# Kernel tuning notes

Hardware: AMD Instinct MI355X
Metric: run time of the kernel (lower is better)

The kernel has to match this reference:

```python
import jax, jax.numpy as jnp
import numpy as np

NEG_SLOPE = 0.2


def gat_layer(x, src, dst, W, att_src, att_dst, bias, n_nodes):
    # PyG GATConv (heads=1): h = x @ W; per-edge logit = LeakyReLU(a_src.h[src] + a_dst.h[dst]);
    # softmax over edges grouped by destination node; out[d] = sum alpha * h[src] + bias.
    h = x @ W                                  # [N, F]
    a_s = h @ att_src                          # [N]
    a_d = h @ att_dst                          # [N]
    e = a_s[src] + a_d[dst]                    # [E]
    e = jnp.where(e > 0, e, NEG_SLOPE * e)     # leaky_relu
    m = jax.ops.segment_max(e, dst, num_segments=n_nodes)   # [N]
    w = jnp.exp(e - m[dst])                    # [E]
    z = jax.ops.segment_sum(w, dst, num_segments=n_nodes)   # [N]
    alpha = w / z[dst]                         # [E] (self-loops guarantee z>0)
    out = jax.ops.segment_sum(alpha[:, None] * h[src], dst, num_segments=n_nodes)
    return out + bias


def setup_inputs() -> dict:
    key = jax.random.key(0)
    ks = jax.random.split(key, 10)
    N, E, C_IN, H1, H2 = 100000, 3200000, 128, 50, 40
    x = jax.random.normal(ks[0], (N, C_IN), dtype=jnp.float32)
    edge_index = jax.random.randint(ks[1], (2, E), 0, N, dtype=jnp.int64)
    g1 = 1.0 / np.sqrt(C_IN)
    g2 = 1.0 / np.sqrt(H1)
    return {
        "x": x,
        "edge_index": edge_index,
        "W1": jax.random.normal(ks[2], (C_IN, H1), dtype=jnp.float32) * g1,
        "att_src1": jax.random.normal(ks[3], (H1,), dtype=jnp.float32) * g2,
        "att_dst1": jax.random.normal(ks[4], (H1,), dtype=jnp.float32) * g2,
        "bias1": jnp.zeros((H1,), dtype=jnp.float32),
        "W2": jax.random.normal(ks[5], (H1, H2), dtype=jnp.float32) * g2,
        "att_src2": jax.random.normal(ks[6], (H2,), dtype=jnp.float32) / np.sqrt(H2),
        "att_dst2": jax.random.normal(ks[7], (H2,), dtype=jnp.float32) / np.sqrt(H2),
        "bias2": jnp.zeros((H2,), dtype=jnp.float32),
    }


def reference(x, edge_index, W1, att_src1, att_dst1, bias1, W2, att_src2, att_dst2, bias2):
    n_nodes = x.shape[0]
    # PyG GATConv default add_self_loops=True: append (i, i) for every node.
    loop = jnp.arange(n_nodes, dtype=edge_index.dtype)
    src = jnp.concatenate([edge_index[0], loop])
    dst = jnp.concatenate([edge_index[1], loop])
    h = jax.nn.relu(gat_layer(x, src, dst, W1, att_src1, att_dst1, bias1, n_nodes))
    h = jax.nn.relu(gat_layer(h, src, dst, W2, att_src2, att_dst2, bias2, n_nodes))
    return h, edge_index
```

## Files before the change

kernel.cpp:

```cpp
#include <hip/hip_runtime.h>
#include <hip/hip_bf16.h>
#include <math.h>

#define NEG_SLOPE 0.2f
#define RBITS 8
#define RNODES 256
#define CHUNK 8192
#define CAP   9216
#define HS    32


__device__ __forceinline__ float waveReduceSum(float v) {
    #pragma unroll
    for (int off = 32; off > 0; off >>= 1) v += __shfl_xor(v, off);
    return v;
}

__device__ __forceinline__ unsigned pack_bf16(float a, float b) {
    __hip_bfloat162 p(__float2bfloat16(a), __float2bfloat16(b));
    return *reinterpret_cast<unsigned*>(&p);
}
__device__ __forceinline__ float bf16lo_f(unsigned u) { return __uint_as_float(u << 16); }
__device__ __forceinline__ float bf16hi_f(unsigned u) { return __uint_as_float(u & 0xFFFF0000u); }


__global__ void prep(const float* __restrict__ W1, float* __restrict__ WT1,
                     const float* __restrict__ W2, float* __restrict__ WT2,
                     int* __restrict__ bcursor,
                     int K1, int F1, int KP1, int FP1,
                     int K2, int F2, int KP2, int FP2, int NB) {
    int i = blockIdx.x * blockDim.x + threadIdx.x;
    int z1 = FP1 * KP1, z2 = FP2 * KP2;
    if (i < z1) {
        int f = i / KP1, k = i - f * KP1;
        WT1[i] = (f < F1 && k < K1) ? W1[k * F1 + f] : 0.f;
    } else if (i < z1 + z2) {
        int j = i - z1;
        int f = j / KP2, k = j - f * KP2;
        WT2[j] = (f < F2 && k < K2) ? W2[k * F2 + f] : 0.f;
    } else if (i < z1 + z2 + NB) {
        bcursor[i - z1 - z2] = 0;
    }
}


__global__ __launch_bounds__(512) void binning(
        const int* __restrict__ src, const int* __restrict__ dst,
        int* __restrict__ bcursor, int* __restrict__ binned,
        long E, int N, long TOT) {
    __shared__ int hist[512];
    __shared__ int base[512];
    int t = threadIdx.x;
    hist[t] = 0;
    __syncthreads();
    long c0 = blockIdx.x * (long)CHUNK;
    long c1 = c0 + CHUNK; if (c1 > TOT) c1 = TOT;
    for (long i = c0 + t; i < c1; i += 512) {
        int d = (i < E) ? dst[i] : (int)(i - E);
        atomicAdd(&hist[d >> RBITS], 1);
    }
    __syncthreads();
    {
        int c = hist[t];
        base[t] = c ? atomicAdd(&bcursor[t], c) : 0;
        hist[t] = 0;
    }
    __syncthreads();
    for (long i = c0 + t; i < c1; i += 512) {
        int s, d;
        if (i < E) { s = src[i]; d = dst[i]; } else { s = d = (int)(i - E); }
        int b = d >> RBITS;
        int p = base[b] + atomicAdd(&hist[b], 1);
        if (p >= CAP) p = CAP - 1;
        binned[(long)b * CAP + p] = ((d & (RNODES - 1)) << 17) | s;
    }
}

__global__ __launch_bounds__(512) void bucket_scan(
        const int* __restrict__ bcursor, int* __restrict__ bstarts,
        int* __restrict__ starts, int NB, int N, int TOT) {
    __shared__ int s[512];
    int t = threadIdx.x;
    int v = (t < NB) ? bcursor[t] : 0;
    s[t] = v;
    __syncthreads();
    for (int off = 1; off < 512; off <<= 1) {
        int u = (t >= off) ? s[t - off] : 0;
        __syncthreads();
        s[t] += u;
        __syncthreads();
    }
    int excl = s[t] - v;
    if (t < NB) bstarts[t] = excl;
    if (t == 0) { bstarts[NB] = TOT; starts[N] = TOT; }
}

__global__ __launch_bounds__(512) void bucket_csr(
        const int* __restrict__ binned, const int* __restrict__ bstarts,
        int* __restrict__ starts, int* __restrict__ csr_src, int N) {
    __shared__ int cnt[RNODES];
    __shared__ int scn[RNODES];
    int b = blockIdx.x, t = threadIdx.x;
    int node0 = b << RBITS;
    int R = N - node0; if (R > RNODES) R = RNODES;
    int e0 = bstarts[b];
    int ecnt = bstarts[b + 1] - e0;
    const int* bin = binned + (long)b * CAP;
    if (t < RNODES) cnt[t] = 0;
    __syncthreads();
    for (int i = t; i < ecnt; i += 512)
        atomicAdd(&cnt[bin[i] >> 17], 1);
    __syncthreads();
    int v = (t < RNODES) ? cnt[t] : 0;
    if (t < RNODES) scn[t] = v;
    __syncthreads();
    for (int off = 1; off < RNODES; off <<= 1) {
        int u = (t >= off && t < RNODES) ? scn[t - off] : 0;
        __syncthreads();
        if (t < RNODES) scn[t] += u;
        __syncthreads();
    }
    if (t < RNODES) {
        int excl = scn[t] - v;
        if (t < R) starts[node0 + t] = e0 + excl;
        cnt[t] = excl;
    }
    __syncthreads();
    for (int i = t; i < ecnt; i += 512) {
        int packed = bin[i];
        int ld = packed >> 17;
        int p = atomicAdd(&cnt[ld], 1);
        csr_src[e0 + p] = packed & 0x1FFFF;
    }
}

template <int K, int KP, int F, int FPH>
__global__ __launch_bounds__(512) void gemm_tile(
        const float* __restrict__ x, const float* __restrict__ WT,
        const float* __restrict__ att_s, const float* __restrict__ att_d,
        unsigned* __restrict__ hb, float* __restrict__ as_, float* __restrict__ ad_,
        int N) {
    __shared__ float xT[KP * 65];
    __shared__ float asl[64], adl[64];
    int t = threadIdx.x;
    int lane = t & 63;
    int w = t >> 6;
    long n0 = (long)blockIdx.x * 64;
    int n = (int)n0 + lane;

    if (t < 64) { asl[t] = 0.f; adl[t] = 0.f; }
    for (int idx = t; idx < KP * 64; idx += 512) {
        int nn = idx / KP, k = idx - nn * KP;
        float v = 0.f;
        if (k < K && n0 + nn < N) v = x[(n0 + nn) * (long)K + k];
        xT[k * 65 + nn] = v;
    }
    __syncthreads();

    int f0 = __builtin_amdgcn_readfirstlane(w * 8);
    float acc[8] = {0.f, 0.f, 0.f, 0.f, 0.f, 0.f, 0.f, 0.f};
    if (f0 < F) {
        const float* wbase = WT + (long)f0 * KP;
        for (int k0 = 0; k0 < KP; k0 += 4) {
            float x0 = xT[(k0 + 0) * 65 + lane];
            float x1 = xT[(k0 + 1) * 65 + lane];
            float x2 = xT[(k0 + 2) * 65 + lane];
            float x3 = xT[(k0 + 3) * 65 + lane];
            #pragma unroll
            for (int j = 0; j < 8; ++j) {
                const float* wr = wbase + j * KP + k0;
                float a = acc[j];
                a = fmaf(wr[0], x0, a);
                a = fmaf(wr[1], x1, a);
                a = fmaf(wr[2], x2, a);
                a = fmaf(wr[3], x3, a);
                acc[j] = a;
            }
        }
        float ps = 0.f, pd = 0.f;
        #pragma unroll
        for (int j = 0; j < 8; ++j) {
            float sa = (f0 + j < F) ? att_s[f0 + j] : 0.f;
            float da = (f0 + j < F) ? att_d[f0 + j] : 0.f;
            ps = fmaf(acc[j], sa, ps);
            pd = fmaf(acc[j], da, pd);
        }
        atomicAdd(&asl[lane], ps);
        atomicAdd(&adl[lane], pd);
    }
    __syncthreads();

    if (f0 < F && n < N) {
        int f0h = f0 >> 1;
        #pragma unroll
        for (int q = 0; q < 4; ++q) {
            int fp = f0h + q;
            if (fp < FPH) hb[(long)n * HS + fp] = pack_bf16(acc[2 * q], acc[2 * q + 1]);
        }
    }
    if (w == 0 && n < N) { as_[n] = asl[lane]; ad_[n] = adl[lane]; }
}

template <int F>
__global__ __launch_bounds__(256) void gat_gather(
                           const int* __restrict__ csr_src, const int* __restrict__ starts,
                           const float* __restrict__ as_, const float* __restrict__ ad_,
                           const unsigned* __restrict__ hb, const float* __restrict__ bias,
                           float* __restrict__ out, int N) {
    constexpr int NU4 = (F + 7) / 8;
    int lane = threadIdx.x & 63;
    int g  = lane >> 3;
    int fl = lane & 7;
    bool actf = (fl < NU4);
    long wave = (blockIdx.x * (long)blockDim.x + threadIdx.x) >> 6;
    if (wave >= N) return;
    int d = (int)wave;
    int s0 = starts[d], s1 = starts[d + 1];
    float add = ad_[d];
    const unsigned* hbase = hb + 4 * fl;

    float lsum = 0.f;
    float a0 = 0.f, a1 = 0.f, a2 = 0.f, a3 = 0.f;
    float a4 = 0.f, a5 = 0.f, a6 = 0.f, a7 = 0.f;

    for (int base = s0; base < s1; base += 64) {
        int k = base + lane;
        int s = (k < s1) ? csr_src[k] : 0;
        unsigned soff = (unsigned)s << 5;
        float e = as_[s] + add;
        e = e > 0.f ? e : NEG_SLOPE * e;
        float w = (k < s1) ? __expf(e) : 0.f;
        lsum += w;
        int cnt = min(64, s1 - base);
        int nst = (cnt + 7) >> 3;
        int j = 0;
        for (; j + 4 <= nst; j += 4) {
            int i0 = 8 * j + g;
            unsigned so0 = __shfl(soff, i0);
            unsigned so1 = __shfl(soff, i0 + 8);
            unsigned so2 = __shfl(soff, i0 + 16);
            unsigned so3 = __shfl(soff, i0 + 24);
            uint4 h0 = make_uint4(0u,0u,0u,0u), h1 = h0, h2 = h0, h3 = h0;
            if (actf) {
                h0 = *(const uint4*)(hbase + so0);
                h1 = *(const uint4*)(hbase + so1);
                h2 = *(const uint4*)(hbase + so2);
                h3 = *(const uint4*)(hbase + so3);
            }
            float w0 = __shfl(w, i0);
            float w1 = __shfl(w, i0 + 8);
            float w2 = __shfl(w, i0 + 16);
            float w3 = __shfl(w, i0 + 24);
            a0 = fmaf(w0, bf16lo_f(h0.x), a0); a1 = fmaf(w0, bf16hi_f(h0.x), a1);
            a2 = fmaf(w0, bf16lo_f(h0.y), a2); a3 = fmaf(w0, bf16hi_f(h0.y), a3);
            a4 = fmaf(w0, bf16lo_f(h0.z), a4); a5 = fmaf(w0, bf16hi_f(h0.z), a5);
            a6 = fmaf(w0, bf16lo_f(h0.w), a6); a7 = fmaf(w0, bf16hi_f(h0.w), a7);
            a0 = fmaf(w1, bf16lo_f(h1.x), a0); a1 = fmaf(w1, bf16hi_f(h1.x), a1);
            a2 = fmaf(w1, bf16lo_f(h1.y), a2); a3 = fmaf(w1, bf16hi_f(h1.y), a3);
            a4 = fmaf(w1, bf16lo_f(h1.z), a4); a5 = fmaf(w1, bf16hi_f(h1.z), a5);
            a6 = fmaf(w1, bf16lo_f(h1.w), a6); a7 = fmaf(w1, bf16hi_f(h1.w), a7);
            a0 = fmaf(w2, bf16lo_f(h2.x), a0); a1 = fmaf(w2, bf16hi_f(h2.x), a1);
            a2 = fmaf(w2, bf16lo_f(h2.y), a2); a3 = fmaf(w2, bf16hi_f(h2.y), a3);
            a4 = fmaf(w2, bf16lo_f(h2.z), a4); a5 = fmaf(w2, bf16hi_f(h2.z), a5);
            a6 = fmaf(w2, bf16lo_f(h2.w), a6); a7 = fmaf(w2, bf16hi_f(h2.w), a7);
            a0 = fmaf(w3, bf16lo_f(h3.x), a0); a1 = fmaf(w3, bf16hi_f(h3.x), a1);
            a2 = fmaf(w3, bf16lo_f(h3.y), a2); a3 = fmaf(w3, bf16hi_f(h3.y), a3);
            a4 = fmaf(w3, bf16lo_f(h3.z), a4); a5 = fmaf(w3, bf16hi_f(h3.z), a5);
            a6 = fmaf(w3, bf16lo_f(h3.w), a6); a7 = fmaf(w3, bf16hi_f(h3.w), a7);
        }
        for (; j < nst; ++j) {
            int idx = 8 * j + g;
            float wp = __shfl(w, idx);
            unsigned so = __shfl(soff, idx);
            if (actf) {
                uint4 hv = *(const uint4*)(hbase + so);
                a0 = fmaf(wp, bf16lo_f(hv.x), a0); a1 = fmaf(wp, bf16hi_f(hv.x), a1);
                a2 = fmaf(wp, bf16lo_f(hv.y), a2); a3 = fmaf(wp, bf16hi_f(hv.y), a3);
                a4 = fmaf(wp, bf16lo_f(hv.z), a4); a5 = fmaf(wp, bf16hi_f(hv.z), a5);
                a6 = fmaf(wp, bf16lo_f(hv.w), a6); a7 = fmaf(wp, bf16hi_f(hv.w), a7);
            }
        }
    }

    #pragma unroll
    for (int off = 8; off < 64; off <<= 1) {
        a0 += __shfl_xor(a0, off); a1 += __shfl_xor(a1, off);
        a2 += __shfl_xor(a2, off); a3 += __shfl_xor(a3, off);
        a4 += __shfl_xor(a4, off); a5 += __shfl_xor(a5, off);
        a6 += __shfl_xor(a6, off); a7 += __shfl_xor(a7, off);
    }
    float l = waveReduceSum(lsum);

    if (actf) {
        float inv = 1.f / l;
        int fb = 8 * fl;
        float v[8] = {a0, a1, a2, a3, a4, a5, a6, a7};
        float2* orow = (float2*)(out + (long)d * F + fb);
        #pragma unroll
        for (int i = 0; i < 8; i += 2) {
            if (fb + i < F) {
                float u0 = v[i]     * inv + bias[fb + i];
                float u1 = v[i + 1] * inv + bias[fb + i + 1];
                u0 = u0 > 0.f ? u0 : 0.f;
                u1 = u1 > 0.f ? u1 : 0.f;
                orow[i >> 1] = make_float2(u0, u1);
            }
        }
    }
}

__global__ void copy_edges4(const int4* __restrict__ ei, float4* __restrict__ out, long n4) {
    long i = blockIdx.x * (long)blockDim.x + threadIdx.x;
    if (i < n4) {
        int4 v = ei[i];
        out[i] = make_float4((float)v.x, (float)v.y, (float)v.z, (float)v.w);
    }
}
__global__ void copy_edges_tail(const int* __restrict__ ei, float* __restrict__ out,
                                long lo, long n) {
    long i = lo + blockIdx.x * (long)blockDim.x + threadIdx.x;
    if (i < n) out[i] = (float)ei[i];
}


extern "C" void kernel_launch(void* const* d_in, const int* in_sizes, int n_in,
                              void* d_out, int out_size, void* d_ws, size_t ws_size,
                              hipStream_t stream) {
    const float* x         = (const float*)d_in[0];
    const int*   edge_idx  = (const int*)d_in[1];
    const float* W1        = (const float*)d_in[2];
    const float* att_src1  = (const float*)d_in[3];
    const float* att_dst1  = (const float*)d_in[4];
    const float* bias1     = (const float*)d_in[5];
    const float* W2        = (const float*)d_in[6];
    const float* att_src2  = (const float*)d_in[7];
    const float* att_dst2  = (const float*)d_in[8];
    const float* bias2     = (const float*)d_in[9];

    const int  CIN = 128, F1 = 50, F2 = 40;
    const int  KP1 = 128, FP1 = 56;
    const int  KP2 = 52,  FP2 = 40;
    const int  N = in_sizes[0] / CIN;
    const long E = in_sizes[1] / 2;
    const int* src = edge_idx;
    const int* dst = edge_idx + E;
    const long TOT = E + N;
    const int  NB = (N + RNODES - 1) >> RBITS;

    char* wsb = (char*)d_ws;
    size_t regionA = (size_t)NB * CAP * 4;
    if ((size_t)N * HS * 4 > regionA) regionA = (size_t)N * HS * 4;
    int*      binned = (int*)wsb;
    unsigned* hb     = (unsigned*)wsb;
    float*    hout   = (float*)(wsb + regionA);
    float*    as_    = hout + (long)N * F1;
    float*    ad_    = as_ + N;
    int*      starts  = (int*)(ad_ + N);
    int*      csr_src = starts + (N + 1);
    int*      bstarts = csr_src + TOT;
    int*      bcursor = bstarts + (NB + 1);
    float*    WT1     = (float*)(bcursor + NB + 3);
    float*    WT2     = WT1 + FP1 * KP1;

    float* out_h = (float*)d_out;
    float* out_e = out_h + (long)N * F2;

    const int B = 256;
    const int nodeWaveBlocks = (N + 3) / 4;
    const int nTileBlocks = (N + 63) / 64;
    const int nBinBlocks = (int)((TOT + CHUNK - 1) / CHUNK);
    const int prepElems = FP1 * KP1 + FP2 * KP2 + NB;

    prep<<<dim3((prepElems + B - 1) / B), dim3(B), 0, stream>>>(
        W1, WT1, W2, WT2, bcursor, CIN, F1, KP1, FP1, F1, F2, KP2, FP2, NB);
    binning<<<dim3(nBinBlocks), dim3(512), 0, stream>>>(src, dst, bcursor, binned, E, N, TOT);
    bucket_scan<<<dim3(1), dim3(512), 0, stream>>>(bcursor, bstarts, starts, NB, N, (int)TOT);
    bucket_csr<<<dim3(NB), dim3(512), 0, stream>>>(binned, bstarts, starts, csr_src, N);

    gemm_tile<CIN, KP1, F1, FP1 / 2><<<dim3(nTileBlocks), dim3(512), 0, stream>>>(x, WT1, att_src1, att_dst1, hb, as_, ad_, N);
    gat_gather<F1><<<dim3(nodeWaveBlocks), dim3(B), 0, stream>>>(csr_src, starts, as_, ad_, hb, bias1, hout, N);

    gemm_tile<F1, KP2, F2, FP2 / 2><<<dim3(nTileBlocks), dim3(512), 0, stream>>>(hout, WT2, att_src2, att_dst2, hb, as_, ad_, N);
    gat_gather<F2><<<dim3(nodeWaveBlocks), dim3(B), 0, stream>>>(csr_src, starts, as_, ad_, hb, bias2, out_h, N);

    long n_e = 2 * E;
    long n4  = n_e / 4;
    copy_edges4<<<dim3((int)((n4 + B - 1) / B)), dim3(B), 0, stream>>>((const int4*)edge_idx, (float4*)out_e, n4);
    if (n_e - n4 * 4 > 0)
        copy_edges_tail<<<dim3(1), dim3(B), 0, stream>>>(edge_idx, out_e, n4 * 4, n_e);
}
```

Measured before the change: 406.5 us.

## Precompute edge weights in separate pass, shrink layer-2 row stride, fuse edge copy into GEMM

```diff
diff --git a/kernel.cpp b/kernel.cpp
--- a/kernel.cpp
+++ b/kernel.cpp
@@ -7,7 +7,8 @@
 #define RNODES 256
 #define CHUNK 8192
 #define CAP   9216
-#define HS    32
+#define HS1   32
+#define HS2   20
 
 
 __device__ __forceinline__ float waveReduceSum(float v) {
@@ -134,12 +135,31 @@
     }
 }
 
-template <int K, int KP, int F, int FPH>
+__global__ __launch_bounds__(256) void edge_w(
+        const int* __restrict__ csr_src, const int* __restrict__ starts,
+        const float* __restrict__ as_, const float* __restrict__ ad_,
+        float* __restrict__ w_, int N) {
+    long wave = (blockIdx.x * (long)blockDim.x + threadIdx.x) >> 6;
+    int lane = threadIdx.x & 63;
+    if (wave >= N) return;
+    int d = (int)wave;
+    int s0 = starts[d], s1 = starts[d + 1];
+    float add = ad_[d];
+    for (int k = s0 + lane; k < s1; k += 64) {
+        int s = csr_src[k];
+        float e = as_[s] + add;
+        e = e > 0.f ? e : NEG_SLOPE * e;
+        w_[k] = __expf(e);
+    }
+}
+
+template <int K, int KP, int F, int FPH, int HS_, bool DOCOPY>
 __global__ __launch_bounds__(512) void gemm_tile(
         const float* __restrict__ x, const float* __restrict__ WT,
         const float* __restrict__ att_s, const float* __restrict__ att_d,
         unsigned* __restrict__ hb, float* __restrict__ as_, float* __restrict__ ad_,
-        int N) {
+        int N, const int4* __restrict__ ei4, float4* __restrict__ oe4,
+        long q0, long q1) {
     __shared__ float xT[KP * 65];
     __shared__ float asl[64], adl[64];
     int t = threadIdx.x;
@@ -195,16 +215,25 @@
         #pragma unroll
         for (int q = 0; q < 4; ++q) {
             int fp = f0h + q;
-            if (fp < FPH) hb[(long)n * HS + fp] = pack_bf16(acc[2 * q], acc[2 * q + 1]);
+            if (fp < FPH) hb[(long)n * HS_ + fp] = pack_bf16(acc[2 * q], acc[2 * q + 1]);
         }
     }
     if (w == 0 && n < N) { as_[n] = asl[lane]; ad_[n] = adl[lane]; }
-}
-
-template <int F>
+
+    if (DOCOPY) {
+        long gtid = (long)blockIdx.x * blockDim.x + threadIdx.x;
+        long stride = (long)gridDim.x * blockDim.x;
+        for (long i = q0 + gtid; i < q1; i += stride) {
+            int4 v = ei4[i];
+            oe4[i] = make_float4((float)v.x, (float)v.y, (float)v.z, (float)v.w);
+        }
+    }
+}
+
+template <int F, int HS_>
 __global__ __launch_bounds__(256) void gat_gather(
                            const int* __restrict__ csr_src, const int* __restrict__ starts,
-                           const float* __restrict__ as_, const float* __restrict__ ad_,
+                           const float* __restrict__ w_,
                            const unsigned* __restrict__ hb, const float* __restrict__ bias,
                            float* __restrict__ out, int N) {
     constexpr int NU4 = (F + 7) / 8;
@@ -216,7 +245,6 @@
     if (wave >= N) return;
     int d = (int)wave;
     int s0 = starts[d], s1 = starts[d + 1];
-    float add = ad_[d];
     const unsigned* hbase = hb + 4 * fl;
 
     float lsum = 0.f;
@@ -226,10 +254,8 @@
     for (int base = s0; base < s1; base += 64) {
         int k = base + lane;
         int s = (k < s1) ? csr_src[k] : 0;
-        unsigned soff = (unsigned)s << 5;
-        float e = as_[s] + add;
-        e = e > 0.f ? e : NEG_SLOPE * e;
-        float w = (k < s1) ? __expf(e) : 0.f;
+        float w = (k < s1) ? w_[k] : 0.f;
+        unsigned soff = (unsigned)s * HS_;
         lsum += w;
         int cnt = min(64, s1 - base);
         int nst = (cnt + 7) >> 3;
@@ -309,13 +335,6 @@
     }
 }
 
-__global__ void copy_edges4(const int4* __restrict__ ei, float4* __restrict__ out, long n4) {
-    long i = blockIdx.x * (long)blockDim.x + threadIdx.x;
-    if (i < n4) {
-        int4 v = ei[i];
-        out[i] = make_float4((float)v.x, (float)v.y, (float)v.z, (float)v.w);
-    }
-}
 __global__ void copy_edges_tail(const int* __restrict__ ei, float* __restrict__ out,
                                 long lo, long n) {
     long i = lo + blockIdx.x * (long)blockDim.x + threadIdx.x;
@@ -349,7 +368,7 @@
 
     char* wsb = (char*)d_ws;
     size_t regionA = (size_t)NB * CAP * 4;
-    if ((size_t)N * HS * 4 > regionA) regionA = (size_t)N * HS * 4;
+    if ((size_t)N * HS1 * 4 > regionA) regionA = (size_t)N * HS1 * 4;
     int*      binned = (int*)wsb;
     unsigned* hb     = (unsigned*)wsb;
     float*    hout   = (float*)(wsb + regionA);
@@ -357,7 +376,8 @@
     float*    ad_    = as_ + N;
     int*      starts  = (int*)(ad_ + N);
     int*      csr_src = starts + (N + 1);
-    int*      bstarts = csr_src + TOT;
+    float*    w_      = (float*)(csr_src + TOT);
+    int*      bstarts = (int*)(w_ + TOT);
     int*      bcursor = bstarts + (NB + 1);
     float*    WT1     = (float*)(bcursor + NB + 3);
     float*    WT2     = WT1 + FP1 * KP1;
@@ -371,21 +391,28 @@
     const int nBinBlocks = (int)((TOT + CHUNK - 1) / CHUNK);
     const int prepElems = FP1 * KP1 + FP2 * KP2 + NB;
 
+    long n_e  = 2 * E;
+    long n4   = n_e / 4;
+    long qmid = n4 / 2;
+
     prep<<<dim3((prepElems + B - 1) / B), dim3(B), 0, stream>>>(
         W1, WT1, W2, WT2, bcursor, CIN, F1, KP1, FP1, F1, F2, KP2, FP2, NB);
     binning<<<dim3(nBinBlocks), dim3(512), 0, stream>>>(src, dst, bcursor, binned, E, N, TOT);
     bucket_scan<<<dim3(1), dim3(512), 0, stream>>>(bcursor, bstarts, starts, NB, N, (int)TOT);
     bucket_csr<<<dim3(NB), dim3(512), 0, stream>>>(binned, bstarts, starts, csr_src, N);
 
-    gemm_tile<CIN, KP1, F1, FP1 / 2><<<dim3(nTileBlocks), dim3(512), 0, stream>>>(x, WT1, att_src1, att_dst1, hb, as_, ad_, N);
-    gat_gather<F1><<<dim3(nodeWaveBlocks), dim3(B), 0, stream>>>(csr_src, starts, as_, ad_, hb, bias1, hout, N);
-
-    gemm_tile<F1, KP2, F2, FP2 / 2><<<dim3(nTileBlocks), dim3(512), 0, stream>>>(hout, WT2, att_src2, att_dst2, hb, as_, ad_, N);
-    gat_gather<F2><<<dim3(nodeWaveBlocks), dim3(B), 0, stream>>>(csr_src, starts, as_, ad_, hb, bias2, out_h, N);
-
-    long n_e = 2 * E;
-    long n4  = n_e / 4;
-    copy_edges4<<<dim3((int)((n4 + B - 1) / B)), dim3(B), 0, stream>>>((const int4*)edge_idx, (float4*)out_e, n4);
+    gemm_tile<CIN, KP1, F1, FP1 / 2, HS1, true><<<dim3(nTileBlocks), dim3(512), 0, stream>>>(
+        x, WT1, att_src1, att_dst1, hb, as_, ad_, N,
+        (const int4*)edge_idx, (float4*)out_e, 0, qmid);
+    edge_w<<<dim3(nodeWaveBlocks), dim3(B), 0, stream>>>(csr_src, starts, as_, ad_, w_, N);
+    gat_gather<F1, HS1><<<dim3(nodeWaveBlocks), dim3(B), 0, stream>>>(csr_src, starts, w_, hb, bias1, hout, N);
+
+    gemm_tile<F1, KP2, F2, HS2, HS2, true><<<dim3(nTileBlocks), dim3(512), 0, stream>>>(
+        hout, WT2, att_src2, att_dst2, hb, as_, ad_, N,
+        (const int4*)edge_idx, (float4*)out_e, qmid, n4);
+    edge_w<<<dim3(nodeWaveBlocks), dim3(B), 0, stream>>>(csr_src, starts, as_, ad_, w_, N);
+    gat_gather<F2, HS2><<<dim3(nodeWaveBlocks), dim3(B), 0, stream>>>(csr_src, starts, w_, hb, bias2, out_h, N);
+
     if (n_e - n4 * 4 > 0)
         copy_edges_tail<<<dim3(1), dim3(B), 0, stream>>>(edge_idx, out_e, n4 * 4, n_e);
 }
```

Result: slower. 437.1 us (+7.5%).

## Embed source attention score into bf16 feature rows and shrink layer-2 row stride

Applied to the files above, without the earlier changes.

```diff
diff --git a/kernel.cpp b/kernel.cpp
--- a/kernel.cpp
+++ b/kernel.cpp
@@ -7,7 +7,8 @@
 #define RNODES 256
 #define CHUNK 8192
 #define CAP   9216
-#define HS    32
+#define HS1   32
+#define HS2   24
 
 
 __device__ __forceinline__ float waveReduceSum(float v) {
@@ -134,12 +135,13 @@
     }
 }
 
-template <int K, int KP, int F, int FPH>
+template <int K, int KP, int F, int FPH, int HS_>
 __global__ __launch_bounds__(512) void gemm_tile(
         const float* __restrict__ x, const float* __restrict__ WT,
         const float* __restrict__ att_s, const float* __restrict__ att_d,
-        unsigned* __restrict__ hb, float* __restrict__ as_, float* __restrict__ ad_,
+        unsigned* __restrict__ hb, float* __restrict__ ad_,
         int N) {
+    constexpr int ASLOT = 4 * ((F + 7) / 8);
     __shared__ float xT[KP * 65];
     __shared__ float asl[64], adl[64];
     int t = threadIdx.x;
@@ -195,23 +197,28 @@
         #pragma unroll
         for (int q = 0; q < 4; ++q) {
             int fp = f0h + q;
-            if (fp < FPH) hb[(long)n * HS + fp] = pack_bf16(acc[2 * q], acc[2 * q + 1]);
-        }
-    }
-    if (w == 0 && n < N) { as_[n] = asl[lane]; ad_[n] = adl[lane]; }
-}
-
-template <int F>
+            if (fp < FPH) hb[(long)n * HS_ + fp] = pack_bf16(acc[2 * q], acc[2 * q + 1]);
+        }
+    }
+    if (w == 0 && n < N) {
+        hb[(long)n * HS_ + ASLOT] = __float_as_uint(asl[lane]);
+        ad_[n] = adl[lane];
+    }
+}
+
+template <int F, int HS_>
 __global__ __launch_bounds__(256) void gat_gather(
                            const int* __restrict__ csr_src, const int* __restrict__ starts,
-                           const float* __restrict__ as_, const float* __restrict__ ad_,
+                           const float* __restrict__ ad_,
                            const unsigned* __restrict__ hb, const float* __restrict__ bias,
                            float* __restrict__ out, int N) {
     constexpr int NU4 = (F + 7) / 8;
+    constexpr int ALANE = NU4;
     int lane = threadIdx.x & 63;
     int g  = lane >> 3;
     int fl = lane & 7;
     bool actf = (fl < NU4);
+    bool loadact = (fl <= NU4);
     long wave = (blockIdx.x * (long)blockDim.x + threadIdx.x) >> 6;
     if (wave >= N) return;
     int d = (int)wave;
@@ -226,11 +233,7 @@
     for (int base = s0; base < s1; base += 64) {
         int k = base + lane;
         int s = (k < s1) ? csr_src[k] : 0;
-        unsigned soff = (unsigned)s << 5;
-        float e = as_[s] + add;
-        e = e > 0.f ? e : NEG_SLOPE * e;
-        float w = (k < s1) ? __expf(e) : 0.f;
-        lsum += w;
+        unsigned soff = (unsigned)s * HS_;
         int cnt = min(64, s1 - base);
         int nst = (cnt + 7) >> 3;
         int j = 0;
@@ -241,39 +244,54 @@
             unsigned so2 = __shfl(soff, i0 + 16);
             unsigned so3 = __shfl(soff, i0 + 24);
             uint4 h0 = make_uint4(0u,0u,0u,0u), h1 = h0, h2 = h0, h3 = h0;
-            if (actf) {
+            if (loadact) {
                 h0 = *(const uint4*)(hbase + so0);
                 h1 = *(const uint4*)(hbase + so1);
                 h2 = *(const uint4*)(hbase + so2);
                 h3 = *(const uint4*)(hbase + so3);
             }
-            float w0 = __shfl(w, i0);
-            float w1 = __shfl(w, i0 + 8);
-            float w2 = __shfl(w, i0 + 16);
-            float w3 = __shfl(w, i0 + 24);
-            a0 = fmaf(w0, bf16lo_f(h0.x), a0); a1 = fmaf(w0, bf16hi_f(h0.x), a1);
-            a2 = fmaf(w0, bf16lo_f(h0.y), a2); a3 = fmaf(w0, bf16hi_f(h0.y), a3);
-            a4 = fmaf(w0, bf16lo_f(h0.z), a4); a5 = fmaf(w0, bf16hi_f(h0.z), a5);
-            a6 = fmaf(w0, bf16lo_f(h0.w), a6); a7 = fmaf(w0, bf16hi_f(h0.w), a7);
-            a0 = fmaf(w1, bf16lo_f(h1.x), a0); a1 = fmaf(w1, bf16hi_f(h1.x), a1);
-            a2 = fmaf(w1, bf16lo_f(h1.y), a2); a3 = fmaf(w1, bf16hi_f(h1.y), a3);
-            a4 = fmaf(w1, bf16lo_f(h1.z), a4); a5 = fmaf(w1, bf16hi_f(h1.z), a5);
-            a6 = fmaf(w1, bf16lo_f(h1.w), a6); a7 = fmaf(w1, bf16hi_f(h1.w), a7);
-            a0 = fmaf(w2, bf16lo_f(h2.x), a0); a1 = fmaf(w2, bf16hi_f(h2.x), a1);
-            a2 = fmaf(w2, bf16lo_f(h2.y), a2); a3 = fmaf(w2, bf16hi_f(h2.y), a3);
-            a4 = fmaf(w2, bf16lo_f(h2.z), a4); a5 = fmaf(w2, bf16hi_f(h2.z), a5);
-            a6 = fmaf(w2, bf16lo_f(h2.w), a6); a7 = fmaf(w2, bf16hi_f(h2.w), a7);
-            a0 = fmaf(w3, bf16lo_f(h3.x), a0); a1 = fmaf(w3, bf16hi_f(h3.x), a1);
-            a2 = fmaf(w3, bf16lo_f(h3.y), a2); a3 = fmaf(w3, bf16hi_f(h3.y), a3);
-            a4 = fmaf(w3, bf16lo_f(h3.z), a4); a5 = fmaf(w3, bf16hi_f(h3.z), a5);
-            a6 = fmaf(w3, bf16lo_f(h3.w), a6); a7 = fmaf(w3, bf16hi_f(h3.w), a7);
+            float e0 = __shfl(__uint_as_float(h0.x), ALANE, 8) + add;
+            float e1 = __shfl(__uint_as_float(h1.x), ALANE, 8) + add;
+            float e2 = __shfl(__uint_as_float(h2.x), ALANE, 8) + add;
+            float e3 = __shfl(__uint_as_float(h3.x), ALANE, 8) + add;
+            e0 = e0 > 0.f ? e0 : NEG_SLOPE * e0;
+            e1 = e1 > 0.f ? e1 : NEG_SLOPE * e1;
+            e2 = e2 > 0.f ? e2 : NEG_SLOPE * e2;
+            e3 = e3 > 0.f ? e3 : NEG_SLOPE * e3;
+            float w0 = (i0      < cnt) ? __expf(e0) : 0.f;
+            float w1 = (i0 + 8  < cnt) ? __expf(e1) : 0.f;
+            float w2 = (i0 + 16 < cnt) ? __expf(e2) : 0.f;
+            float w3 = (i0 + 24 < cnt) ? __expf(e3) : 0.f;
+            lsum += w0 + w1 + w2 + w3;
+            if (actf) {
+                a0 = fmaf(w0, bf16lo_f(h0.x), a0); a1 = fmaf(w0, bf16hi_f(h0.x), a1);
+                a2 = fmaf(w0, bf16lo_f(h0.y), a2); a3 = fmaf(w0, bf16hi_f(h0.y), a3);
+                a4 = fmaf(w0, bf16lo_f(h0.z), a4); a5 = fmaf(w0, bf16hi_f(h0.z), a5);
+                a6 = fmaf(w0, bf16lo_f(h0.w), a6); a7 = fmaf(w0, bf16hi_f(h0.w), a7);
+                a0 = fmaf(w1, bf16lo_f(h1.x), a0); a1 = fmaf(w1, bf16hi_f(h1.x), a1);
+                a2 = fmaf(w1, bf16lo_f(h1.y), a2); a3 = fmaf(w1, bf16hi_f(h1.y), a3);
+                a4 = fmaf(w1, bf16lo_f(h1.z), a4); a5 = fmaf(w1, bf16hi_f(h1.z), a5);
+                a6 = fmaf(w1, bf16lo_f(h1.w), a6); a7 = fmaf(w1, bf16hi_f(h1.w), a7);
+                a0 = fmaf(w2, bf16lo_f(h2.x), a0); a1 = fmaf(w2, bf16hi_f(h2.x), a1);
+                a2 = fmaf(w2, bf16lo_f(h2.y), a2); a3 = fmaf(w2, bf16hi_f(h2.y), a3);
+                a4 = fmaf(w2, bf16lo_f(h2.z), a4); a5 = fmaf(w2, bf16hi_f(h2.z), a5);
+                a6 = fmaf(w2, bf16lo_f(h2.w), a6); a7 = fmaf(w2, bf16hi_f(h2.w), a7);
+                a0 = fmaf(w3, bf16lo_f(h3.x), a0); a1 = fmaf(w3, bf16hi_f(h3.x), a1);
+                a2 = fmaf(w3, bf16lo_f(h3.y), a2); a3 = fmaf(w3, bf16hi_f(h3.y), a3);
+                a4 = fmaf(w3, bf16lo_f(h3.z), a4); a5 = fmaf(w3, bf16hi_f(h3.z), a5);
+                a6 = fmaf(w3, bf16lo_f(h3.w), a6); a7 = fmaf(w3, bf16hi_f(h3.w), a7);
+            }
         }
         for (; j < nst; ++j) {
             int idx = 8 * j + g;
-            float wp = __shfl(w, idx);
             unsigned so = __shfl(soff, idx);
+            uint4 hv = make_uint4(0u,0u,0u,0u);
+            if (loadact) hv = *(const uint4*)(hbase + so);
+            float e = __shfl(__uint_as_float(hv.x), ALANE, 8) + add;
+            e = e > 0.f ? e : NEG_SLOPE * e;
+            float wp = (idx < cnt) ? __expf(e) : 0.f;
+            lsum += wp;
             if (actf) {
-                uint4 hv = *(const uint4*)(hbase + so);
                 a0 = fmaf(wp, bf16lo_f(hv.x), a0); a1 = fmaf(wp, bf16hi_f(hv.x), a1);
                 a2 = fmaf(wp, bf16lo_f(hv.y), a2); a3 = fmaf(wp, bf16hi_f(hv.y), a3);
                 a4 = fmaf(wp, bf16lo_f(hv.z), a4); a5 = fmaf(wp, bf16hi_f(hv.z), a5);
@@ -292,7 +310,7 @@
     float l = waveReduceSum(lsum);
 
     if (actf) {
-        float inv = 1.f / l;
+        float inv = 8.f / l;
         int fb = 8 * fl;
         float v[8] = {a0, a1, a2, a3, a4, a5, a6, a7};
         float2* orow = (float2*)(out + (long)d * F + fb);
@@ -349,12 +367,11 @@
 
     char* wsb = (char*)d_ws;
     size_t regionA = (size_t)NB * CAP * 4;
-    if ((size_t)N * HS * 4 > regionA) regionA = (size_t)N * HS * 4;
+    if ((size_t)N * HS1 * 4 > regionA) regionA = (size_t)N * HS1 * 4;
     int*      binned = (int*)wsb;
     unsigned* hb     = (unsigned*)wsb;
     float*    hout   = (float*)(wsb + regionA);
-    float*    as_    = hout + (long)N * F1;
-    float*    ad_    = as_ + N;
+    float*    ad_    = hout + (long)N * F1;
     int*      starts  = (int*)(ad_ + N);
     int*      csr_src = starts + (N + 1);
     int*      bstarts = csr_src + TOT;
@@ -377,11 +394,15 @@
     bucket_scan<<<dim3(1), dim3(512), 0, stream>>>(bcursor, bstarts, starts, NB, N, (int)TOT);
     bucket_csr<<<dim3(NB), dim3(512), 0, stream>>>(binned, bstarts, starts, csr_src, N);
 
-    gemm_tile<CIN, KP1, F1, FP1 / 2><<<dim3(nTileBlocks), dim3(512), 0, stream>>>(x, WT1, att_src1, att_dst1, hb, as_, ad_, N);
-    gat_gather<F1><<<dim3(nodeWaveBlocks), dim3(B), 0, stream>>>(csr_src, starts, as_, ad_, hb, bias1, hout, N);
-
-    gemm_tile<F1, KP2, F2, FP2 / 2><<<dim3(nTileBlocks), dim3(512), 0, stream>>>(hout, WT2, att_src2, att_dst2, hb, as_, ad_, N);
-    gat_gather<F2><<<dim3(nodeWaveBlocks), dim3(B), 0, stream>>>(csr_src, starts, as_, ad_, hb, bias2, out_h, N);
+    gemm_tile<CIN, KP1, F1, FP1 / 2, HS1><<<dim3(nTileBlocks), dim3(512), 0, stream>>>(
+        x, WT1, att_src1, att_dst1, hb, ad_, N);
+    gat_gather<F1, HS1><<<dim3(nodeWaveBlocks), dim3(B), 0, stream>>>(
+        csr_src, starts, ad_, hb, bias1, hout, N);
+
+    gemm_tile<F1, KP2, F2, FP2 / 2, HS2><<<dim3(nTileBlocks), dim3(512), 0, stream>>>(
+        hout, WT2, att_src2, att_dst2, hb, ad_, N);
+    gat_gather<F2, HS2><<<dim3(nodeWaveBlocks), dim3(B), 0, stream>>>(
+        csr_src, starts, ad_, hb, bias2, out_h, N);
 
     long n_e = 2 * E;
     long n4  = n_e / 4;
```

After: 443.8 us. 1.09x slower.

## Precompute per-edge attention weights in separate kernel; shrink layer-2 bf16 row stride

Applied to the files above, without the earlier changes.

```diff
diff --git a/kernel.cpp b/kernel.cpp
--- a/kernel.cpp
+++ b/kernel.cpp
@@ -7,7 +7,8 @@
 #define RNODES 256
 #define CHUNK 8192
 #define CAP   9216
-#define HS    32
+#define HS1   32
+#define HS2   20
 
 
 __device__ __forceinline__ float waveReduceSum(float v) {
@@ -134,7 +135,25 @@
     }
 }
 
-template <int K, int KP, int F, int FPH>
+__global__ __launch_bounds__(256) void edge_w(
+        const int* __restrict__ csr_src, const int* __restrict__ starts,
+        const float* __restrict__ as_, const float* __restrict__ ad_,
+        float* __restrict__ w_, int N) {
+    int t = blockIdx.x * blockDim.x + threadIdx.x;
+    int node = t >> 4;
+    int l = t & 15;
+    if (node >= N) return;
+    int s0 = starts[node], s1 = starts[node + 1];
+    float add = ad_[node];
+    for (int k = s0 + l; k < s1; k += 16) {
+        int s = csr_src[k];
+        float e = as_[s] + add;
+        e = e > 0.f ? e : NEG_SLOPE * e;
+        w_[k] = __expf(e);
+    }
+}
+
+template <int K, int KP, int F, int FPH, int HS_>
 __global__ __launch_bounds__(512) void gemm_tile(
         const float* __restrict__ x, const float* __restrict__ WT,
         const float* __restrict__ att_s, const float* __restrict__ att_d,
@@ -195,16 +214,16 @@
         #pragma unroll
         for (int q = 0; q < 4; ++q) {
             int fp = f0h + q;
-            if (fp < FPH) hb[(long)n * HS + fp] = pack_bf16(acc[2 * q], acc[2 * q + 1]);
+            if (fp < FPH) hb[(long)n * HS_ + fp] = pack_bf16(acc[2 * q], acc[2 * q + 1]);
         }
     }
     if (w == 0 && n < N) { as_[n] = asl[lane]; ad_[n] = adl[lane]; }
 }
 
-template <int F>
+template <int F, int HS_>
 __global__ __launch_bounds__(256) void gat_gather(
                            const int* __restrict__ csr_src, const int* __restrict__ starts,
-                           const float* __restrict__ as_, const float* __restrict__ ad_,
+                           const float* __restrict__ w_,
                            const unsigned* __restrict__ hb, const float* __restrict__ bias,
                            float* __restrict__ out, int N) {
     constexpr int NU4 = (F + 7) / 8;
@@ -216,7 +235,6 @@
     if (wave >= N) return;
     int d = (int)wave;
     int s0 = starts[d], s1 = starts[d + 1];
-    float add = ad_[d];
     const unsigned* hbase = hb + 4 * fl;
 
     float lsum = 0.f;
@@ -226,10 +244,8 @@
     for (int base = s0; base < s1; base += 64) {
         int k = base + lane;
         int s = (k < s1) ? csr_src[k] : 0;
-        unsigned soff = (unsigned)s << 5;
-        float e = as_[s] + add;
-        e = e > 0.f ? e : NEG_SLOPE * e;
-        float w = (k < s1) ? __expf(e) : 0.f;
+        float w = (k < s1) ? w_[k] : 0.f;
+        unsigned soff = (unsigned)s * HS_;
         lsum += w;
         int cnt = min(64, s1 - base);
         int nst = (cnt + 7) >> 3;
@@ -349,7 +365,7 @@
 
     char* wsb = (char*)d_ws;
     size_t regionA = (size_t)NB * CAP * 4;
-    if ((size_t)N * HS * 4 > regionA) regionA = (size_t)N * HS * 4;
+    if ((size_t)N * HS1 * 4 > regionA) regionA = (size_t)N * HS1 * 4;
     int*      binned = (int*)wsb;
     unsigned* hb     = (unsigned*)wsb;
     float*    hout   = (float*)(wsb + regionA);
@@ -357,7 +373,8 @@
     float*    ad_    = as_ + N;
     int*      starts  = (int*)(ad_ + N);
     int*      csr_src = starts + (N + 1);
-    int*      bstarts = csr_src + TOT;
+    float*    w_      = (float*)(csr_src + TOT);
+    int*      bstarts = (int*)(w_ + TOT);
     int*      bcursor = bstarts + (NB + 1);
     float*    WT1     = (float*)(bcursor + NB + 3);
     float*    WT2     = WT1 + FP1 * KP1;
@@ -367,6 +384,7 @@
 
     const int B = 256;
     const int nodeWaveBlocks = (N + 3) / 4;
+    const int edgeWBlocks = (N * 16 + B - 1) / B;
     const int nTileBlocks = (N + 63) / 64;
     const int nBinBlocks = (int)((TOT + CHUNK - 1) / CHUNK);
     const int prepElems = FP1 * KP1 + FP2 * KP2 + NB;
@@ -377,11 +395,17 @@
     bucket_scan<<<dim3(1), dim3(512), 0, stream>>>(bcursor, bstarts, starts, NB, N, (int)TOT);
     bucket_csr<<<dim3(NB), dim3(512), 0, stream>>>(binned, bstarts, starts, csr_src, N);
 
-    gemm_tile<CIN, KP1, F1, FP1 / 2><<<dim3(nTileBlocks), dim3(512), 0, stream>>>(x, WT1, att_src1, att_dst1, hb, as_, ad_, N);
-    gat_gather<F1><<<dim3(nodeWaveBlocks), dim3(B), 0, stream>>>(csr_src, starts, as_, ad_, hb, bias1, hout, N);
-
-    gemm_tile<F1, KP2, F2, FP2 / 2><<<dim3(nTileBlocks), dim3(512), 0, stream>>>(hout, WT2, att_src2, att_dst2, hb, as_, ad_, N);
-    gat_gather<F2><<<dim3(nodeWaveBlocks), dim3(B), 0, stream>>>(csr_src, starts, as_, ad_, hb, bias2, out_h, N);
+    gemm_tile<CIN, KP1, F1, FP1 / 2, HS1><<<dim3(nTileBlocks), dim3(512), 0, stream>>>(
+        x, WT1, att_src1, att_dst1, hb, as_, ad_, N);
+    edge_w<<<dim3(edgeWBlocks), dim3(B), 0, stream>>>(csr_src, starts, as_, ad_, w_, N);
+    gat_gather<F1, HS1><<<dim3(nodeWaveBlocks), dim3(B), 0, stream>>>(
+        csr_src, starts, w_, hb, bias1, hout, N);
+
+    gemm_tile<F1, KP2, F2, HS2, HS2><<<dim3(nTileBlocks), dim3(512), 0, stream>>>(
+        hout, WT2, att_src2, att_dst2, hb, as_, ad_, N);
+    edge_w<<<dim3(edgeWBlocks), dim3(B), 0, stream>>>(csr_src, starts, as_, ad_, w_, N);
+    gat_gather<F2, HS2><<<dim3(nodeWaveBlocks), dim3(B), 0, stream>>>(
+        csr_src, starts, w_, hb, bias2, out_h, N);
 
     long n_e = 2 * E;
     long n4  = n_e / 4;
```

Measured after the change: 434.3 us. +6.8%, slower.
